# Kernel optimization log

Measured on AMD Instinct MI355X. Metric: run time of the kernel, lower is better.

The kernel has to match this reference:

```python
import jax, jax.numpy as jnp
import numpy as np

B, S, T = 64, 512, 32
H2 = 1024          # hidden_size * 2
ATT = 512          # attention_size


def setup_inputs() -> dict:
    key = jax.random.key(0)
    k1, k2, k3, k4, k5, k6 = jax.random.split(key, 6)
    h = jax.random.normal(k1, (B, S, H2), dtype=jnp.float32)
    h_mask = jax.random.randint(k2, (B, S), 0, 2).astype(jnp.int32)
    ht = jax.random.normal(k3, (B, T, H2), dtype=jnp.float32)
    # Linear params (xavier-ish scale)
    w1_w = jax.random.normal(k4, (ATT, 2 * H2), dtype=jnp.float32) * (1.0 / np.sqrt(2 * H2))
    w1_b = jax.random.normal(k5, (ATT,), dtype=jnp.float32) * 0.02
    u_w = jax.random.normal(k6, (1, ATT), dtype=jnp.float32) * (1.0 / np.sqrt(ATT))
    return {"h": h, "h_mask": h_mask, "ht": ht, "w1_w": w1_w, "w1_b": w1_b, "u_w": u_w}


def reference(h, h_mask, ht, w1_w, w1_b, u_w):
    # h: [B,S,2H], ht: [B,T,2H], h_mask: [B,S] (1 = valid, 0 = pad)
    valid = h_mask != 0                                  # [B,S]
    ht_mean = jnp.mean(ht, axis=1, keepdims=True)        # [B,1,2H]
    h_cat = jnp.concatenate(
        [h, jnp.broadcast_to(ht_mean, h.shape)], axis=2)  # [B,S,4H]
    h_cat = jnp.where(valid[..., None], h_cat, 0.0)
    a = jnp.tanh(jnp.einsum('bsf,af->bsa', h_cat, w1_w) + w1_b)  # [B,S,ATT]
    a = jnp.where(valid[..., None], a, 0.0)
    beta = jnp.einsum('bsa,a->bs', a, u_w[0])            # [B,S]
    beta = jnp.where(valid, beta, -1e20)
    alpha = jax.nn.softmax(beta, axis=1)                 # [B,S]
    s = jnp.einsum('bs,bsd->bd', alpha, h)               # [B,2H]
    return s
```

## Files before the change

kernel.cpp:

```cpp
#include <hip/hip_runtime.h>
#include <math.h>
#include <stdint.h>

#define Bb 64
#define Ss 512
#define Tt 32
#define H2 1024
#define FF 2048
#define ATT 512
#define MM (Bb * Ss)

typedef short bf8 __attribute__((ext_vector_type(8)));
typedef float f4 __attribute__((ext_vector_type(4)));

__device__ __forceinline__ unsigned short f2bf(float f) {
    unsigned u = __float_as_uint(f);
    u = (u + 0x7fffu + ((u >> 16) & 1u)) >> 16;
    return (unsigned short)u;
}

__device__ __forceinline__ void gl_lds16(const void* g, void* l) {
    __builtin_amdgcn_global_load_lds((const __attribute__((address_space(1))) void*)g,
                                     (__attribute__((address_space(3))) void*)l, 16, 0, 0);
}

__device__ __forceinline__ float tanh_fast(float x) {
    return 1.0f - 2.0f / (__expf(2.0f * x) + 1.0f);
}

__global__ void init_kernel(float* __restrict__ beta, float* __restrict__ out) {
    int i = blockIdx.x * 256 + threadIdx.x;
    if (i < Bb * Ss) beta[i] = 0.0f;
    if (i < Bb * H2) out[i] = 0.0f;
}

__global__ void mean_kernel(const float* __restrict__ ht, float* __restrict__ ht_mean) {
    int b = blockIdx.x;
    int d4 = threadIdx.x;
    const float4* p = (const float4*)(ht + (size_t)b * Tt * H2);
    float4 acc = make_float4(0.f, 0.f, 0.f, 0.f);
    #pragma unroll 4
    for (int t = 0; t < Tt; ++t) {
        float4 v = p[(size_t)t * (H2 / 4) + d4];
        acc.x += v.x; acc.y += v.y; acc.z += v.z; acc.w += v.w;
    }
    const float inv = 1.0f / (float)Tt;
    acc.x *= inv; acc.y *= inv; acc.z *= inv; acc.w *= inv;
    ((float4*)(ht_mean + (size_t)b * H2))[d4] = acc;
}

__global__ __launch_bounds__(256) void c2_kernel2(const float* __restrict__ ht_mean,
                                                  const float* __restrict__ w1_w,
                                                  const float* __restrict__ w1_b,
                                                  float* __restrict__ c2) {
    __shared__ float hm[H2];
    int b = blockIdx.x;
    for (int i = threadIdx.x; i < H2; i += 256) hm[i] = ht_mean[(size_t)b * H2 + i];
    __syncthreads();
    int a = blockIdx.y * 64 + ((int)threadIdx.x >> 2);
    int q = (int)threadIdx.x & 3;
    const float4* w   = (const float4*)(w1_w + (size_t)a * FF + H2 + q * 256);
    const float4* hm4 = (const float4*)(hm + q * 256);
    float acc = 0.f;
    #pragma unroll 8
    for (int k = 0; k < 64; ++k) {
        float4 wv = w[k]; float4 hv = hm4[k];
        acc += wv.x * hv.x + wv.y * hv.y + wv.z * hv.z + wv.w * hv.w;
    }
    acc += __shfl_xor(acc, 1);
    acc += __shfl_xor(acc, 2);
    if (q == 0) c2[(size_t)b * ATT + a] = acc + w1_b[a];
}

__global__ void convw_kernel(const float* __restrict__ w1_w, unsigned short* __restrict__ out) {
    size_t e = ((size_t)blockIdx.x * 256 + threadIdx.x) * 8;
    int row = (int)(e >> 10);
    int c = (int)(e & 1023);
    const float* src = w1_w + (size_t)row * FF + c;
    float4 a = *(const float4*)(src);
    float4 b = *(const float4*)(src + 4);
    bf8 v = { (short)f2bf(a.x), (short)f2bf(a.y), (short)f2bf(a.z), (short)f2bf(a.w),
              (short)f2bf(b.x), (short)f2bf(b.y), (short)f2bf(b.z), (short)f2bf(b.w) };
    *(bf8*)(out + e) = v;
}

__global__ __launch_bounds__(256, 3) void gemm_fused3_kernel(
        const float* __restrict__ h, const unsigned short* __restrict__ wb,
        const float* __restrict__ c2, const float* __restrict__ u_w,
        float* __restrict__ beta) {
    __shared__ __align__(16) unsigned short As[2][128 * 32];
    __shared__ __align__(16) unsigned short Bs[2][128 * 32];

    const int id = (int)blockIdx.x;
    const int wg = (id & 7) * 128 + (id >> 3);
    const int mt = wg >> 2, nt = wg & 3;
    const int m0 = mt * 128, n0 = nt * 128;

    const int tid = (int)threadIdx.x;
    const int wid = tid >> 6, lane = tid & 63;
    const int wr = (wid >> 1) * 64, wc = (wid & 1) * 64;
    const int col = lane & 15, rg = lane >> 4;
    const int rswz = rg ^ ((col >> 1) & 3);

    f4 acc[4][4] = {};

    const int arow = tid >> 1;
    const int ako  = (tid & 1) * 2;
    const int aswz = (arow >> 1) & 3;
    const float* Ag = h + (size_t)(m0 + arow) * H2 + ako * 8;
    const int a_off0 = arow * 32 + ((ako    ) ^ aswz) * 8;
    const int a_off1 = arow * 32 + ((ako + 1) ^ aswz) * 8;

    const int brow = tid >> 2;
    const int bsrc = (tid & 3) ^ ((tid >> 3) & 3);
    const unsigned short* Bg = wb + (size_t)(n0 + brow) * H2 + bsrc * 8;
    const int b_ldsbase = wid * 512;

    gl_lds16(Bg,                   &Bs[0][b_ldsbase]);
    gl_lds16(Bg + (size_t)64 * H2, &Bs[0][b_ldsbase + 2048]);
    {
        float4 q0 = *(const float4*)(Ag);
        float4 q1 = *(const float4*)(Ag + 4);
        float4 q2 = *(const float4*)(Ag + 8);
        float4 q3 = *(const float4*)(Ag + 12);
        bf8 c0 = { (short)f2bf(q0.x), (short)f2bf(q0.y), (short)f2bf(q0.z), (short)f2bf(q0.w),
                   (short)f2bf(q1.x), (short)f2bf(q1.y), (short)f2bf(q1.z), (short)f2bf(q1.w) };
        bf8 c1 = { (short)f2bf(q2.x), (short)f2bf(q2.y), (short)f2bf(q2.z), (short)f2bf(q2.w),
                   (short)f2bf(q3.x), (short)f2bf(q3.y), (short)f2bf(q3.z), (short)f2bf(q3.w) };
        *(bf8*)&As[0][a_off0] = c0;
        *(bf8*)&As[0][a_off1] = c1;
    }
    __syncthreads();

    int cur = 0;
    for (int t = 0; t < 32; ++t) {
        float4 q0, q1, q2, q3;
        if (t < 31) {
            const int kn = (t + 1) * 32;
            gl_lds16(Bg + kn,                   &Bs[cur ^ 1][b_ldsbase]);
            gl_lds16(Bg + kn + (size_t)64 * H2, &Bs[cur ^ 1][b_ldsbase + 2048]);
            q0 = *(const float4*)(Ag + kn);
            q1 = *(const float4*)(Ag + kn + 4);
            q2 = *(const float4*)(Ag + kn + 8);
            q3 = *(const float4*)(Ag + kn + 12);
        }
        bf8 av[4], bv[4];
        #pragma unroll
        for (int i = 0; i < 4; ++i) {
            av[i] = *(const bf8*)&As[cur][(wr + i * 16 + col) * 32 + rswz * 8];
            bv[i] = *(const bf8*)&Bs[cur][(wc + i * 16 + col) * 32 + rswz * 8];
        }
        #pragma unroll
        for (int i = 0; i < 4; ++i)
            #pragma unroll
            for (int j = 0; j < 4; ++j)
                acc[i][j] = __builtin_amdgcn_mfma_f32_16x16x32_bf16(av[i], bv[j], acc[i][j], 0, 0, 0);
        if (t < 31) {
            bf8 c0 = { (short)f2bf(q0.x), (short)f2bf(q0.y), (short)f2bf(q0.z), (short)f2bf(q0.w),
                       (short)f2bf(q1.x), (short)f2bf(q1.y), (short)f2bf(q1.z), (short)f2bf(q1.w) };
            bf8 c1 = { (short)f2bf(q2.x), (short)f2bf(q2.y), (short)f2bf(q2.z), (short)f2bf(q2.w),
                       (short)f2bf(q3.x), (short)f2bf(q3.y), (short)f2bf(q3.z), (short)f2bf(q3.w) };
            *(bf8*)&As[cur ^ 1][a_off0] = c0;
            *(bf8*)&As[cur ^ 1][a_off1] = c1;
        }
        __syncthreads();
        cur ^= 1;
    }

    const int b_idx = mt >> 2;
    const float* c2b = c2 + (size_t)b_idx * ATT + n0 + wc;
    const float* ub  = u_w + n0 + wc;
    float rp[4][4] = {};
    #pragma unroll
    for (int j = 0; j < 4; ++j) {
        int n = j * 16 + col;
        float cv = c2b[n];
        float uv = ub[n];
        #pragma unroll
        for (int i = 0; i < 4; ++i)
            #pragma unroll
            for (int r = 0; r < 4; ++r)
                rp[i][r] += tanh_fast(acc[i][j][r] + cv) * uv;
    }
    #pragma unroll
    for (int i = 0; i < 4; ++i)
        #pragma unroll
        for (int r = 0; r < 4; ++r) {
            float v = rp[i][r];
            v += __shfl_xor(v, 1);
            v += __shfl_xor(v, 2);
            v += __shfl_xor(v, 4);
            v += __shfl_xor(v, 8);
            if (col == 0)
                atomicAdd(&beta[(size_t)m0 + wr + i * 16 + rg * 4 + r], v);
        }
}

__global__ void softmax_kernel(const float* __restrict__ beta, const int* __restrict__ h_mask,
                               float* __restrict__ alpha) {
    __shared__ float red[16];
    int b = blockIdx.x;
    int s = (int)threadIdx.x;
    float v = (h_mask[(size_t)b * Ss + s] != 0) ? beta[(size_t)b * Ss + s] : -1e20f;
    float m = v;
    #pragma unroll
    for (int off = 32; off >= 1; off >>= 1) m = fmaxf(m, __shfl_xor(m, off, 64));
    int wave = s >> 6;
    if ((s & 63) == 0) red[wave] = m;
    __syncthreads();
    float mx = red[0];
    #pragma unroll
    for (int w = 1; w < 8; ++w) mx = fmaxf(mx, red[w]);
    float e = expf(v - mx);
    float sum = e;
    #pragma unroll
    for (int off = 32; off >= 1; off >>= 1) sum += __shfl_xor(sum, off, 64);
    __syncthreads();
    if ((s & 63) == 0) red[8 + wave] = sum;
    __syncthreads();
    float tot = 0.f;
    #pragma unroll
    for (int w = 0; w < 8; ++w) tot += red[8 + w];
    alpha[(size_t)b * Ss + s] = e / tot;
}

__global__ void wsum_kernel(const float* __restrict__ h, const float* __restrict__ alpha,
                            float* __restrict__ out) {
    int b = blockIdx.x;
    int d = blockIdx.y * 256 + (int)threadIdx.x;
    int s0 = blockIdx.z * 128;
    const float* hp = h + (size_t)b * Ss * H2 + (size_t)s0 * H2 + d;
    const float* ap = alpha + (size_t)b * Ss + s0;
    float acc = 0.f;
    #pragma unroll 4
    for (int s = 0; s < 128; ++s) acc = fmaf(ap[s], hp[(size_t)s * H2], acc);
    atomicAdd(&out[(size_t)b * H2 + d], acc);
}

extern "C" void kernel_launch(void* const* d_in, const int* in_sizes, int n_in,
                              void* d_out, int out_size, void* d_ws, size_t ws_size,
                              hipStream_t stream) {
    const float* h      = (const float*)d_in[0];
    const int*   h_mask = (const int*)d_in[1];
    const float* ht     = (const float*)d_in[2];
    const float* w1_w   = (const float*)d_in[3];
    const float* w1_b   = (const float*)d_in[4];
    const float* u_w    = (const float*)d_in[5];
    float* out = (float*)d_out;

    float* ws      = (float*)d_ws;
    float* ht_mean = ws;
    float* c2      = ws + 65536;
    float* beta    = ws + 98304;
    float* alpha   = ws + 131072;
    unsigned short* w1a_bf = (unsigned short*)(ws + 164864);

    hipLaunchKernelGGL(init_kernel, dim3(256), dim3(256), 0, stream, beta, out);
    hipLaunchKernelGGL(mean_kernel, dim3(Bb), dim3(256), 0, stream, ht, ht_mean);
    hipLaunchKernelGGL(c2_kernel2, dim3(Bb, 8), dim3(256), 0, stream, ht_mean, w1_w, w1_b, c2);
    hipLaunchKernelGGL(convw_kernel, dim3(256), dim3(256), 0, stream, w1_w, w1a_bf);
    hipLaunchKernelGGL(gemm_fused3_kernel, dim3((MM / 128) * (ATT / 128)), dim3(256), 0, stream,
                       h, w1a_bf, c2, u_w, beta);
    hipLaunchKernelGGL(softmax_kernel, dim3(Bb), dim3(512), 0, stream, beta, h_mask, alpha);
    hipLaunchKernelGGL(wsum_kernel, dim3(Bb, H2 / 256, 4), dim3(256), 0, stream, h, alpha, out);
}
```

Baseline: 301.8 us.

## Pre-convert h to bf16 once and stream both GEMM operands via direct LDS loads

Adds a standalone kernel that converts all of h to bf16 in workspace. The GEMM then loads both A and B tiles through global_load_lds with the same swizzle, dropping the per-tile fp32 loads and in-loop conversions, and raises the occupancy hint to 4. The weighted-sum kernel also reads the bf16 copy, halving its traffic for h. This costs an extra full pass over h (read fp32, write bf16) and lowers the precision of the final weighted sum, since h is now rounded to bf16 there.

```diff
diff --git a/kernel.cpp b/kernel.cpp
--- a/kernel.cpp
+++ b/kernel.cpp
@@ -84,8 +84,17 @@
     *(bf8*)(out + e) = v;
 }
 
-__global__ __launch_bounds__(256, 3) void gemm_fused3_kernel(
-        const float* __restrict__ h, const unsigned short* __restrict__ wb,
+__global__ void convh_kernel(const float* __restrict__ in, unsigned short* __restrict__ out) {
+    size_t i = ((size_t)blockIdx.x * 256 + threadIdx.x) * 8;
+    float4 a = *(const float4*)(in + i);
+    float4 b = *(const float4*)(in + i + 4);
+    bf8 v = { (short)f2bf(a.x), (short)f2bf(a.y), (short)f2bf(a.z), (short)f2bf(a.w),
+              (short)f2bf(b.x), (short)f2bf(b.y), (short)f2bf(b.z), (short)f2bf(b.w) };
+    *(bf8*)(out + i) = v;
+}
+
+__global__ __launch_bounds__(256, 4) void gemm_m97_kernel(
+        const unsigned short* __restrict__ hb, const unsigned short* __restrict__ wb,
         const float* __restrict__ c2, const float* __restrict__ u_w,
         float* __restrict__ beta) {
     __shared__ __align__(16) unsigned short As[2][128 * 32];
@@ -104,46 +113,28 @@
 
     f4 acc[4][4] = {};
 
-    const int arow = tid >> 1;
-    const int ako  = (tid & 1) * 2;
-    const int aswz = (arow >> 1) & 3;
-    const float* Ag = h + (size_t)(m0 + arow) * H2 + ako * 8;
-    const int a_off0 = arow * 32 + ((ako    ) ^ aswz) * 8;
-    const int a_off1 = arow * 32 + ((ako + 1) ^ aswz) * 8;
-
-    const int brow = tid >> 2;
-    const int bsrc = (tid & 3) ^ ((tid >> 3) & 3);
-    const unsigned short* Bg = wb + (size_t)(n0 + brow) * H2 + bsrc * 8;
-    const int b_ldsbase = wid * 512;
-
-    gl_lds16(Bg,                   &Bs[0][b_ldsbase]);
-    gl_lds16(Bg + (size_t)64 * H2, &Bs[0][b_ldsbase + 2048]);
-    {
-        float4 q0 = *(const float4*)(Ag);
-        float4 q1 = *(const float4*)(Ag + 4);
-        float4 q2 = *(const float4*)(Ag + 8);
-        float4 q3 = *(const float4*)(Ag + 12);
-        bf8 c0 = { (short)f2bf(q0.x), (short)f2bf(q0.y), (short)f2bf(q0.z), (short)f2bf(q0.w),
-                   (short)f2bf(q1.x), (short)f2bf(q1.y), (short)f2bf(q1.z), (short)f2bf(q1.w) };
-        bf8 c1 = { (short)f2bf(q2.x), (short)f2bf(q2.y), (short)f2bf(q2.z), (short)f2bf(q2.w),
-                   (short)f2bf(q3.x), (short)f2bf(q3.y), (short)f2bf(q3.z), (short)f2bf(q3.w) };
-        *(bf8*)&As[0][a_off0] = c0;
-        *(bf8*)&As[0][a_off1] = c1;
-    }
+    const int srow = tid >> 2;
+    const int sslot = (tid & 3) ^ ((tid >> 3) & 3);
+    const unsigned short* Agl = hb + (size_t)(m0 + srow) * H2 + sslot * 8;
+    const unsigned short* Bgl = wb + (size_t)(n0 + srow) * H2 + sslot * 8;
+    const int ldsb = wid * 512;
+
+    gl_lds16(Agl,                   &As[0][ldsb]);
+    gl_lds16(Agl + (size_t)64 * H2, &As[0][ldsb + 2048]);
+    gl_lds16(Bgl,                   &Bs[0][ldsb]);
+    gl_lds16(Bgl + (size_t)64 * H2, &Bs[0][ldsb + 2048]);
     __syncthreads();
 
     int cur = 0;
     for (int t = 0; t < 32; ++t) {
-        float4 q0, q1, q2, q3;
         if (t < 31) {
             const int kn = (t + 1) * 32;
-            gl_lds16(Bg + kn,                   &Bs[cur ^ 1][b_ldsbase]);
-            gl_lds16(Bg + kn + (size_t)64 * H2, &Bs[cur ^ 1][b_ldsbase + 2048]);
-            q0 = *(const float4*)(Ag + kn);
-            q1 = *(const float4*)(Ag + kn + 4);
-            q2 = *(const float4*)(Ag + kn + 8);
-            q3 = *(const float4*)(Ag + kn + 12);
-        }
+            gl_lds16(Agl + kn,                   &As[cur ^ 1][ldsb]);
+            gl_lds16(Agl + kn + (size_t)64 * H2, &As[cur ^ 1][ldsb + 2048]);
+            gl_lds16(Bgl + kn,                   &Bs[cur ^ 1][ldsb]);
+            gl_lds16(Bgl + kn + (size_t)64 * H2, &Bs[cur ^ 1][ldsb + 2048]);
+        }
+        __builtin_amdgcn_sched_barrier(0);
         bf8 av[4], bv[4];
         #pragma unroll
         for (int i = 0; i < 4; ++i) {
@@ -155,14 +146,6 @@
             #pragma unroll
             for (int j = 0; j < 4; ++j)
                 acc[i][j] = __builtin_amdgcn_mfma_f32_16x16x32_bf16(av[i], bv[j], acc[i][j], 0, 0, 0);
-        if (t < 31) {
-            bf8 c0 = { (short)f2bf(q0.x), (short)f2bf(q0.y), (short)f2bf(q0.z), (short)f2bf(q0.w),
-                       (short)f2bf(q1.x), (short)f2bf(q1.y), (short)f2bf(q1.z), (short)f2bf(q1.w) };
-            bf8 c1 = { (short)f2bf(q2.x), (short)f2bf(q2.y), (short)f2bf(q2.z), (short)f2bf(q2.w),
-                       (short)f2bf(q3.x), (short)f2bf(q3.y), (short)f2bf(q3.z), (short)f2bf(q3.w) };
-            *(bf8*)&As[cur ^ 1][a_off0] = c0;
-            *(bf8*)&As[cur ^ 1][a_off1] = c1;
-        }
         __syncthreads();
         cur ^= 1;
     }
@@ -224,17 +207,29 @@
     alpha[(size_t)b * Ss + s] = e / tot;
 }
 
-__global__ void wsum_kernel(const float* __restrict__ h, const float* __restrict__ alpha,
-                            float* __restrict__ out) {
-    int b = blockIdx.x;
-    int d = blockIdx.y * 256 + (int)threadIdx.x;
-    int s0 = blockIdx.z * 128;
-    const float* hp = h + (size_t)b * Ss * H2 + (size_t)s0 * H2 + d;
+__global__ void wsum_bf_kernel(const unsigned short* __restrict__ hb,
+                               const float* __restrict__ alpha, float* __restrict__ out) {
+    int b = blockIdx.x;
+    int g = (int)threadIdx.x >> 7;
+    int t = (int)threadIdx.x & 127;
+    int d0 = t * 8;
+    int s0 = blockIdx.y * 64 + g * 32;
+    const unsigned short* hp = hb + (size_t)b * Ss * H2 + (size_t)s0 * H2 + d0;
     const float* ap = alpha + (size_t)b * Ss + s0;
-    float acc = 0.f;
+    float acc[8] = {};
     #pragma unroll 4
-    for (int s = 0; s < 128; ++s) acc = fmaf(ap[s], hp[(size_t)s * H2], acc);
-    atomicAdd(&out[(size_t)b * H2 + d], acc);
+    for (int s = 0; s < 32; ++s) {
+        bf8 v = *(const bf8*)(hp + (size_t)s * H2);
+        float a = ap[s];
+        #pragma unroll
+        for (int j = 0; j < 8; ++j) {
+            float hv = __uint_as_float(((unsigned)(unsigned short)v[j]) << 16);
+            acc[j] = fmaf(a, hv, acc[j]);
+        }
+    }
+    #pragma unroll
+    for (int j = 0; j < 8; ++j)
+        atomicAdd(&out[(size_t)b * H2 + d0 + j], acc[j]);
 }
 
 extern "C" void kernel_launch(void* const* d_in, const int* in_sizes, int n_in,
@@ -253,14 +248,16 @@
     float* c2      = ws + 65536;
     float* beta    = ws + 98304;
     float* alpha   = ws + 131072;
-    unsigned short* w1a_bf = (unsigned short*)(ws + 164864);
+    unsigned short* w1a_bf = (unsigned short*)((char*)d_ws + 659456);
+    unsigned short* h_bf   = (unsigned short*)((char*)d_ws + 659456 + 1048576);
 
     hipLaunchKernelGGL(init_kernel, dim3(256), dim3(256), 0, stream, beta, out);
     hipLaunchKernelGGL(mean_kernel, dim3(Bb), dim3(256), 0, stream, ht, ht_mean);
     hipLaunchKernelGGL(c2_kernel2, dim3(Bb, 8), dim3(256), 0, stream, ht_mean, w1_w, w1_b, c2);
     hipLaunchKernelGGL(convw_kernel, dim3(256), dim3(256), 0, stream, w1_w, w1a_bf);
-    hipLaunchKernelGGL(gemm_fused3_kernel, dim3((MM / 128) * (ATT / 128)), dim3(256), 0, stream,
-                       h, w1a_bf, c2, u_w, beta);
+    hipLaunchKernelGGL(convh_kernel, dim3(16384), dim3(256), 0, stream, h, h_bf);
+    hipLaunchKernelGGL(gemm_m97_kernel, dim3((MM / 128) * (ATT / 128)), dim3(256), 0, stream,
+                       h_bf, w1a_bf, c2, u_w, beta);
     hipLaunchKernelGGL(softmax_kernel, dim3(Bb), dim3(512), 0, stream, beta, h_mask, alpha);
-    hipLaunchKernelGGL(wsum_kernel, dim3(Bb, H2 / 256, 4), dim3(256), 0, stream, h, alpha, out);
-}
+    hipLaunchKernelGGL(wsum_bf_kernel, dim3(Bb, 8), dim3(256), 0, stream, h_bf, alpha, out);
+}
```

New measurement: 336.5 us. +11.5%, slower.
